# Performance work log

Measured on AMD Instinct MI355X. Metric: run time of the kernel, lower is better.

The kernel has to match this reference:

```python
import jax, jax.numpy as jnp
import numpy as np

N_NODES = 100000
N_EDGES = 3200000
F_IN = 128
CHANNELS = 128


def setup_inputs() -> dict:
    key = jax.random.key(0)
    k1, k2, k3, k4, k5 = jax.random.split(key, 5)
    x = jax.random.normal(k1, (N_NODES, F_IN), dtype=jnp.float32)
    kernel = jax.random.normal(k2, (F_IN, CHANNELS), dtype=jnp.float32) * (1.0 / np.sqrt(F_IN))
    bias = jnp.zeros((CHANNELS,), dtype=jnp.float32)
    edge_row = jnp.sort(jax.random.randint(k3, (N_EDGES,), 0, N_NODES, dtype=jnp.int32))
    edge_col = jax.random.randint(k4, (N_EDGES,), 0, N_NODES, dtype=jnp.int32)
    edge_val = jax.random.uniform(k5, (N_EDGES,), dtype=jnp.float32)
    return {"x": x, "kernel": kernel, "bias": bias, "edge_val": edge_val,
            "edge_row": edge_row, "edge_col": edge_col}


def reference(x, kernel, bias, edge_val, edge_row, edge_col):
    # Z = relu(A_tilde @ (X @ W) + b), A_tilde given in COO form (row, col, val)
    n = x.shape[0]
    xw = x @ kernel                              # [N, C] dense projection
    msgs = xw[edge_col] * edge_val[:, None]      # [E, C] gather + scale
    agg = jax.ops.segment_sum(msgs, edge_row, num_segments=n)  # SpMM scatter
    return jax.nn.relu(agg + bias)
```

## Files before the change

kernel.cpp:

```cpp
#include <hip/hip_runtime.h>

#define F_IN 128
#define CH   128

typedef __attribute__((ext_vector_type(8))) short bf16x8;
typedef __attribute__((ext_vector_type(4))) float f32x4;
typedef __attribute__((ext_vector_type(2))) float f32x2;
typedef __attribute__((ext_vector_type(2))) unsigned u32x2;

static __device__ __forceinline__ ushort f2b(float f) {
  union { float f; unsigned u; } v; v.f = f;
  const unsigned u = v.u;
  return (ushort)((u + 0x7FFFu + ((u >> 16) & 1u)) >> 16);
}

__global__ __launch_bounds__(512) void gemm_rowptr_fused(
    const float* __restrict__ x, const float* __restrict__ w,
    unsigned char* __restrict__ xwq, float* __restrict__ scale,
    const int* __restrict__ edge_row, int* __restrict__ row_ptr,
    int n, int n_edges, int gemm_blocks) {
  __shared__ __align__(16) ushort Wt[F_IN * CH];
  const int t = threadIdx.x;

  if ((int)blockIdx.x >= gemm_blocks) {
    const int base = (((int)blockIdx.x - gemm_blocks) * 512 + t) * 4;
    if (base < n_edges) {
      const int4 er = *(const int4*)&edge_row[base];
      const int nxt = (base + 4 < n_edges) ? edge_row[base + 4] : n;
      if (base == 0) {
        for (int r = 0; r <= er.x; ++r) row_ptr[r] = 0;
      }
      for (int r = er.x + 1; r <= er.y; ++r) row_ptr[r] = base + 1;
      for (int r = er.y + 1; r <= er.z; ++r) row_ptr[r] = base + 2;
      for (int r = er.z + 1; r <= er.w; ++r) row_ptr[r] = base + 3;
      for (int r = er.w + 1; r <= nxt;  ++r) row_ptr[r] = base + 4;
    }
    return;
  }

  for (int i = t; i < (F_IN * CH) / 4; i += 512) {
    const int k  = i >> 5;
    const int n4 = (i & 31) << 2;
    const f32x4 wv = *(const f32x4*)&w[k * CH + n4];
#pragma unroll
    for (int q = 0; q < 4; ++q) {
      const int nn = n4 + q;
      const int byte = (nn * 256 + k * 2) ^ ((nn & 7) << 4);
      *(ushort*)((char*)Wt + byte) = f2b(wv[q]);
    }
  }
  __syncthreads();

  const int wave = t >> 6, lane = t & 63;
  const int li   = lane & 15;
  const int kgrp = (lane >> 4) * 8;
  const int R0   = blockIdx.x * 128 + wave * 16;
  const int arow = R0 + li;

  bf16x8 a[4];
#pragma unroll
  for (int s = 0; s < 4; ++s) {
    if (arow < n) {
      const f32x4 p0 = __builtin_nontemporal_load(
          (const f32x4*)&x[arow * F_IN + s * 32 + kgrp]);
      const f32x4 p1 = __builtin_nontemporal_load(
          (const f32x4*)&x[arow * F_IN + s * 32 + kgrp + 4]);
#pragma unroll
      for (int j = 0; j < 4; ++j) {
        a[s][j]     = (short)f2b(p0[j]);
        a[s][j + 4] = (short)f2b(p1[j]);
      }
    } else {
#pragma unroll
      for (int j = 0; j < 8; ++j) a[s][j] = (short)0;
    }
  }

  f32x4 acc[8];
#pragma unroll
  for (int t8 = 0; t8 < 8; ++t8) acc[t8] = (f32x4){0.f, 0.f, 0.f, 0.f};

#pragma unroll
  for (int t8 = 0; t8 < 8; ++t8) {
    const int col = t8 * 16 + li;
#pragma unroll
    for (int s = 0; s < 4; ++s) {
      const int byte = (col * 256 + (s * 32 + kgrp) * 2) ^ ((col & 7) << 4);
      const bf16x8 b = *(const bf16x8*)((const char*)Wt + byte);
      acc[t8] = __builtin_amdgcn_mfma_f32_16x16x32_bf16(a[s], b, acc[t8], 0, 0, 0);
    }
  }

  float inv4[4];
  const int r0 = R0 + (lane >> 4) * 4;
#pragma unroll
  for (int i = 0; i < 4; ++i) {
    float m = 0.f;
#pragma unroll
    for (int t8 = 0; t8 < 8; ++t8) m = fmaxf(m, fabsf(acc[t8][i]));
    m = fmaxf(m, __shfl_xor(m, 1));
    m = fmaxf(m, __shfl_xor(m, 2));
    m = fmaxf(m, __shfl_xor(m, 4));
    m = fmaxf(m, __shfl_xor(m, 8));
    inv4[i] = (m > 1e-20f) ? 127.f / m : 0.f;
    const int rr = r0 + i;
    if (rr < n && li == 0) scale[rr] = m * (1.f / 127.f);
  }

  __syncthreads();
  unsigned char* qb8 = (unsigned char*)Wt + wave * 2048;
#pragma unroll
  for (int i = 0; i < 4; ++i) {
    const int rl = (lane >> 4) * 4 + i;
#pragma unroll
    for (int t8 = 0; t8 < 8; ++t8) {
      const float q = rintf(acc[t8][i] * inv4[i]) + 128.f;
      qb8[rl * 128 + t8 * 16 + li] = (unsigned char)q;
    }
  }
#pragma unroll
  for (int p = 0; p < 4; ++p) {
    const int idx = p * 64 + lane;
    const int rl  = idx >> 4;
    const int off = (idx & 15) * 8;
    const int rrow = blockIdx.x * 128 + wave * 16 + rl;
    if (rrow < n) {
      const u32x2 v = *(const u32x2*)&qb8[rl * 128 + off];
      *(u32x2*)&xwq[(size_t)rrow * CH + off] = v;
    }
  }
}

#define ACCD(word, j0, vv)                                                \
  do {                                                                    \
    f32x2 lo_, hi_;                                                       \
    lo_[0] = (float)((word) & 0xFFu);                                     \
    lo_[1] = (float)(((word) >> 8) & 0xFFu);                              \
    hi_[0] = (float)(((word) >> 16) & 0xFFu);                             \
    hi_[1] = (float)((word) >> 24);                                       \
    acc2[(j0)]     = __builtin_elementwise_fma(vv, lo_, acc2[(j0)]);      \
    acc2[(j0) + 1] = __builtin_elementwise_fma(vv, hi_, acc2[(j0) + 1]);  \
  } while (0)

#define ACC8PK(U, V)                                                      \
  do {                                                                    \
    const f32x2 vv_ = {(V), (V)};                                         \
    ACCD((U)[0], 0, vv_);                                                 \
    ACCD((U)[1], 2, vv_);                                                 \
  } while (0)

__global__ __launch_bounds__(256, 4) void spmm_qwave(
    const unsigned char* __restrict__ xwq, const float* __restrict__ scale,
    const float* __restrict__ edge_val, const int* __restrict__ edge_col,
    const int* __restrict__ row_ptr, const float* __restrict__ bias,
    float* __restrict__ out, int n) {
  __shared__ int   cbuf[16 * 40];
  __shared__ float vbuf[16 * 40];
  const int tid = threadIdx.x;
  const int row = (int)((blockIdx.x * 256 + tid) >> 4);
  if (row >= n) return;
  const int li = tid & 15;
  const int qb = (tid >> 4) * 40;
  const u32x2* __restrict__ xw2 = (const u32x2*)xwq;

  const int start = row_ptr[row], end = row_ptr[row + 1];

  f32x2 acc2[4];
#pragma unroll
  for (int j = 0; j < 4; ++j) acc2[j] = (f32x2){0.f, 0.f};
  float S = 0.f;

  for (int e0 = start; e0 < end; e0 += 32) {
    const int ea = e0 + li, eb = e0 + 16 + li;
    int   c0 = 0, c1 = 0;
    float v0 = 0.f, v1 = 0.f;
    if (ea < end) {
      c0 = __builtin_nontemporal_load(edge_col + ea);
      v0 = __builtin_nontemporal_load(edge_val + ea) * scale[c0];
    }
    if (eb < end) {
      c1 = __builtin_nontemporal_load(edge_col + eb);
      v1 = __builtin_nontemporal_load(edge_val + eb) * scale[c1];
    }
    S += v0 + v1;
    cbuf[qb + li] = c0;  cbuf[qb + 16 + li] = c1;
    vbuf[qb + li] = v0;  vbuf[qb + 16 + li] = v1;

    u32x2 u[32];
#pragma unroll
    for (int it4 = 0; it4 < 8; ++it4) {
      const int4 c4 = *(const int4*)&cbuf[qb + it4 * 4];
      u[it4 * 4 + 0] = xw2[c4.x * 16 + li];
      u[it4 * 4 + 1] = xw2[c4.y * 16 + li];
      u[it4 * 4 + 2] = xw2[c4.z * 16 + li];
      u[it4 * 4 + 3] = xw2[c4.w * 16 + li];
    }

    __builtin_amdgcn_sched_barrier(0);

#pragma unroll
    for (int g = 0; g < 4; ++g) {
      if (e0 + g * 8 >= end) break;
      const f32x4 va = *(const f32x4*)&vbuf[qb + g * 8];
      const f32x4 vb = *(const f32x4*)&vbuf[qb + g * 8 + 4];
      ACC8PK(u[g * 8 + 0], va[0]);
      ACC8PK(u[g * 8 + 1], va[1]);
      ACC8PK(u[g * 8 + 2], va[2]);
      ACC8PK(u[g * 8 + 3], va[3]);
      ACC8PK(u[g * 8 + 4], vb[0]);
      ACC8PK(u[g * 8 + 5], vb[1]);
      ACC8PK(u[g * 8 + 6], vb[2]);
      ACC8PK(u[g * 8 + 7], vb[3]);
    }
  }

  S += __shfl_xor(S, 1);
  S += __shfl_xor(S, 2);
  S += __shfl_xor(S, 4);
  S += __shfl_xor(S, 8);

  const float off = 128.f * S;
  const float* a = (const float*)acc2;
  const int cb = li * 8;
  const f32x4 b0 = *(const f32x4*)&bias[cb];
  const f32x4 b1 = *(const f32x4*)&bias[cb + 4];
  f32x4 o0, o1;
  o0[0] = fmaxf(a[0] - off + b0[0], 0.f);
  o0[1] = fmaxf(a[1] - off + b0[1], 0.f);
  o0[2] = fmaxf(a[2] - off + b0[2], 0.f);
  o0[3] = fmaxf(a[3] - off + b0[3], 0.f);
  o1[0] = fmaxf(a[4] - off + b1[0], 0.f);
  o1[1] = fmaxf(a[5] - off + b1[1], 0.f);
  o1[2] = fmaxf(a[6] - off + b1[2], 0.f);
  o1[3] = fmaxf(a[7] - off + b1[3], 0.f);
  __builtin_nontemporal_store(o0, (f32x4*)&out[(size_t)row * CH + cb]);
  __builtin_nontemporal_store(o1, (f32x4*)&out[(size_t)row * CH + cb + 4]);
}

extern "C" void kernel_launch(void* const* d_in, const int* in_sizes, int n_in,
                              void* d_out, int out_size, void* d_ws, size_t ws_size,
                              hipStream_t stream) {
  const float* x        = (const float*)d_in[0];
  const float* kernel   = (const float*)d_in[1];
  const float* bias     = (const float*)d_in[2];
  const float* edge_val = (const float*)d_in[3];
  const int*   edge_row = (const int*)d_in[4];
  const int*   edge_col = (const int*)d_in[5];
  float* out = (float*)d_out;

  const int n       = in_sizes[0] / F_IN;
  const int n_edges = in_sizes[3];

  unsigned char* xwq = (unsigned char*)d_ws;
  float* scale = (float*)((char*)d_ws + (size_t)n * CH);
  int* rowptr  = (int*)((char*)d_ws + (size_t)n * CH + (size_t)n * sizeof(float));

  const int GB = (n + 127) / 128;
  const int RB = (n_edges / 4 + 511) / 512;
  gemm_rowptr_fused<<<GB + RB, 512, 0, stream>>>(x, kernel, xwq, scale,
                                                 edge_row, rowptr,
                                                 n, n_edges, GB);

  const int blocks = (n * 16 + 255) / 256;
  spmm_qwave<<<blocks, 256, 0, stream>>>(xwq, scale, edge_val, edge_col,
                                         rowptr, bias, out, n);
}
```

Before: 106.6 us.

## Gather quantized rows into LDS via global_load_lds instead of register loads

Replaces the register-based gather of 32 neighbor rows per iteration with direct global-to-LDS loads (global_load_lds, 16 bytes per lane) of 16 neighbor rows into a per-wave 8 KB staging buffer, then reads them back from LDS for the FMA accumulation. The aim is to cut register pressure from the 32-element u array and allow higher occupancy, since the launch-bounds occupancy hint is removed. In exchange it adds a full vmcnt(0) wait each iteration, halves edges per iteration, and uses 32 KB of LDS per block, which may itself limit occupancy and serialize load and compute.

```diff
diff --git a/kernel.cpp b/kernel.cpp
--- a/kernel.cpp
+++ b/kernel.cpp
@@ -149,19 +149,25 @@
     ACCD((U)[1], 2, vv_);                                                 \
   } while (0)
 
-__global__ __launch_bounds__(256, 4) void spmm_qwave(
+__global__ __launch_bounds__(256) void spmm_glds(
     const unsigned char* __restrict__ xwq, const float* __restrict__ scale,
     const float* __restrict__ edge_val, const int* __restrict__ edge_col,
     const int* __restrict__ row_ptr, const float* __restrict__ bias,
     float* __restrict__ out, int n) {
-  __shared__ int   cbuf[16 * 40];
-  __shared__ float vbuf[16 * 40];
-  const int tid = threadIdx.x;
-  const int row = (int)((blockIdx.x * 256 + tid) >> 4);
+  __shared__ __align__(16) unsigned char stage[4][8192];
+  __shared__ int   cbuf[16 * 20];
+  __shared__ float vbuf[16 * 20];
+  const int tid  = threadIdx.x;
+  const int wv   = tid >> 6;
+  const int lane = tid & 63;
+  const int row  = (int)((blockIdx.x * 256 + tid) >> 4);
   if (row >= n) return;
-  const int li = tid & 15;
-  const int qb = (tid >> 4) * 40;
-  const u32x2* __restrict__ xw2 = (const u32x2*)xwq;
+  const int q     = lane >> 4;
+  const int li    = lane & 15;
+  const int qslab = (tid >> 4) * 20;
+  const int kk_hi = li >> 3;
+  const int chunk = lane & 7;
+  unsigned char* wstage = stage[wv];
 
   const int start = row_ptr[row], end = row_ptr[row + 1];
 
@@ -170,47 +176,39 @@
   for (int j = 0; j < 4; ++j) acc2[j] = (f32x2){0.f, 0.f};
   float S = 0.f;
 
-  for (int e0 = start; e0 < end; e0 += 32) {
-    const int ea = e0 + li, eb = e0 + 16 + li;
-    int   c0 = 0, c1 = 0;
-    float v0 = 0.f, v1 = 0.f;
-    if (ea < end) {
-      c0 = __builtin_nontemporal_load(edge_col + ea);
-      v0 = __builtin_nontemporal_load(edge_val + ea) * scale[c0];
-    }
-    if (eb < end) {
-      c1 = __builtin_nontemporal_load(edge_col + eb);
-      v1 = __builtin_nontemporal_load(edge_val + eb) * scale[c1];
-    }
-    S += v0 + v1;
-    cbuf[qb + li] = c0;  cbuf[qb + 16 + li] = c1;
-    vbuf[qb + li] = v0;  vbuf[qb + 16 + li] = v1;
-
-    u32x2 u[32];
-#pragma unroll
-    for (int it4 = 0; it4 < 8; ++it4) {
-      const int4 c4 = *(const int4*)&cbuf[qb + it4 * 4];
-      u[it4 * 4 + 0] = xw2[c4.x * 16 + li];
-      u[it4 * 4 + 1] = xw2[c4.y * 16 + li];
-      u[it4 * 4 + 2] = xw2[c4.z * 16 + li];
-      u[it4 * 4 + 3] = xw2[c4.w * 16 + li];
-    }
-
+  for (int e0 = start; e0 < end; e0 += 16) {
+    const int e = e0 + li;
+    int   c_my = 0;
+    float vp_my = 0.f;
+    if (e < end) {
+      c_my = __builtin_nontemporal_load(edge_col + e);
+      vp_my = __builtin_nontemporal_load(edge_val + e) * scale[c_my];
+    }
+    S += vp_my;
+    cbuf[qslab + li] = c_my;
+    vbuf[qslab + li] = vp_my;
+
+#pragma unroll
+    for (int i = 0; i < 8; ++i) {
+      const int c = cbuf[qslab + i * 2 + kk_hi];
+      __builtin_amdgcn_global_load_lds(
+          (const unsigned*)(xwq + (size_t)c * 128 + chunk * 16),
+          (unsigned*)(wstage + i * 1024), 16, 0, 0);
+    }
+    asm volatile("s_waitcnt vmcnt(0)" ::: "memory");
     __builtin_amdgcn_sched_barrier(0);
 
 #pragma unroll
-    for (int g = 0; g < 4; ++g) {
-      if (e0 + g * 8 >= end) break;
-      const f32x4 va = *(const f32x4*)&vbuf[qb + g * 8];
-      const f32x4 vb = *(const f32x4*)&vbuf[qb + g * 8 + 4];
-      ACC8PK(u[g * 8 + 0], va[0]);
-      ACC8PK(u[g * 8 + 1], va[1]);
-      ACC8PK(u[g * 8 + 2], va[2]);
-      ACC8PK(u[g * 8 + 3], va[3]);
-      ACC8PK(u[g * 8 + 4], vb[0]);
-      ACC8PK(u[g * 8 + 5], vb[1]);
-      ACC8PK(u[g * 8 + 6], vb[2]);
-      ACC8PK(u[g * 8 + 7], vb[3]);
+    for (int g4 = 0; g4 < 4; ++g4) {
+      if (e0 + g4 * 4 >= end) break;
+      const f32x4 v4 = *(const f32x4*)&vbuf[qslab + g4 * 4];
+#pragma unroll
+      for (int kk = 0; kk < 4; ++kk) {
+        const int k = g4 * 4 + kk;
+        const u32x2 u = *(const u32x2*)&wstage[(k >> 1) * 1024 + q * 256 +
+                                               (k & 1) * 128 + li * 8];
+        ACC8PK(u, v4[kk]);
+      }
     }
   }
 
@@ -262,6 +260,6 @@
                                                  n, n_edges, GB);
 
   const int blocks = (n * 16 + 255) / 256;
-  spmm_qwave<<<blocks, 256, 0, stream>>>(xwq, scale, edge_val, edge_col,
-                                         rowptr, bias, out, n);
-}
+  spmm_glds<<<blocks, 256, 0, stream>>>(xwq, scale, edge_val, edge_col,
+                                        rowptr, bias, out, n);
+}
```

After: 107.5 us. No clear change (+0.9%).
